# Kernel tuning notes

Measured on AMD Instinct MI355X. Metric: run time of the kernel, lower is better.

The kernel has to match this reference:

```python
import jax, jax.numpy as jnp
import numpy as np

B, L, D_MODEL, HEADS, EXP, DEPTH = 2, 2048, 1024, 16, 2, 12
D_EXP = D_MODEL * EXP
D_HEAD = D_EXP // HEADS


def _layernorm(x, g, b, eps=1e-5):
    mu = jnp.mean(x, axis=-1, keepdims=True)
    var = jnp.mean(jnp.square(x - mu), axis=-1, keepdims=True)
    return (x - mu) * jax.lax.rsqrt(var + eps) * g + b


def setup_inputs() -> dict:
    key = jax.random.key(0)
    ks = jax.random.split(key, 4)
    x = jax.random.normal(ks[0], (B, L, D_MODEL), dtype=jnp.float32)
    w_in = jax.random.normal(ks[1], (D_MODEL, 4 * D_EXP), dtype=jnp.float32) * 0.02
    w_out = jax.random.normal(ks[2], (D_EXP, D_MODEL), dtype=jnp.float32) * (0.02 / np.sqrt(2 * DEPTH))
    return {
        "x": x,
        "ln1_g": jnp.ones((D_MODEL,), jnp.float32),
        "ln1_b": jnp.zeros((D_MODEL,), jnp.float32),
        "ln2_g": jnp.ones((D_MODEL,), jnp.float32),
        "ln2_b": jnp.zeros((D_MODEL,), jnp.float32),
        "w_in": w_in,
        "w_out": w_out,
        "smear_factor": jnp.linspace(-6.0, 6.0, HEADS, dtype=jnp.float32),
        "log_scale": jnp.zeros((HEADS,), jnp.float32),
    }


def reference(x, ln1_g, ln1_b, ln2_g, ln2_b, w_in, w_out, smear_factor, log_scale):
    b, l, d = x.shape
    h = smear_factor.shape[0]
    d_exp = w_in.shape[1] // 4
    dh = d_exp // h

    qkvp = _layernorm(x, ln1_g, ln1_b) @ w_in  # [b, l, 4*d_exp]
    q, k, v, p = jnp.split(qkvp, 4, axis=-1)
    # 'b i (h d) -> b h i d'
    to_heads = lambda t: t.reshape(b, l, h, dh).transpose(0, 2, 1, 3)
    q, k, v = to_heads(q), to_heads(k), to_heads(v)

    # smeared keys: k_i <- (1-s)*k_i + s*k_{i-1}  (zero at i=0)
    smear = jax.nn.sigmoid(smear_factor)[None, :, None, None]
    k_prev = jnp.pad(k, ((0, 0), (0, 0), (1, 0), (0, 0)))[:, :, :-1, :]
    k = (1.0 - smear) * k + smear * k_prev

    # ALiBi-style additive mask: slope[h]*j on causal part, -1e10 above diag
    half = h // 2
    slopes = jnp.concatenate([2.0 ** jnp.linspace(0.0, -8.0, half), jnp.zeros((h - half,), jnp.float32)])
    j = jnp.arange(l)
    causal = jnp.where(j[None, :] > j[:, None], jnp.float32(-1e10), jnp.float32(0.0))  # [l, l]
    mask = slopes[:, None, None] * j[None, None, :].astype(jnp.float32) + causal[None, :, :]  # [h, l, l]

    # SDPA with q/s, k/s and default scale 1/sqrt(dh): logits = q k^T / (s^2 sqrt(dh))
    inv = 1.0 / (jnp.exp(2.0 * log_scale)[None, :, None, None] * jnp.sqrt(jnp.float32(dh)))
    logits = jnp.einsum('bhid,bhjd->bhij', q, k) * inv + mask[None]
    attn = jax.nn.softmax(logits, axis=-1)
    o = jnp.einsum('bhij,bhjd->bhid', attn, v)
    o = o.transpose(0, 2, 1, 3).reshape(b, l, h * dh)  # 'b h i d -> b i (h d)'

    out = (jax.nn.silu(p) * o) @ w_out
    return _layernorm(out, ln2_g, ln2_b)
```

## Files before the change

kernel.cpp:

```cpp
#include <hip/hip_runtime.h>

typedef unsigned short u16;
typedef __attribute__((ext_vector_type(8))) short bf16x8;
typedef __attribute__((ext_vector_type(8))) unsigned short u16x8;
typedef __attribute__((ext_vector_type(4))) float f32x4;

#define L_SEQ 2048
#define NTOK 4096
#define DMODEL 1024
#define DEXP 2048
#define NH 16
#define DH 128

__device__ __forceinline__ u16 f2bf(float f) {
    unsigned u = __float_as_uint(f);
    unsigned r = (u + 0x7FFFu + ((u >> 16) & 1u)) >> 16;
    return (u16)r;
}
__device__ __forceinline__ float bf2f(u16 h) {
    return __uint_as_float(((unsigned)h) << 16);
}

template <int CTRL>
__device__ __forceinline__ float dpp_f(float x) {
    return __int_as_float(__builtin_amdgcn_update_dpp(0, __float_as_int(x), CTRL, 0xF, 0xF, true));
}
__device__ __forceinline__ float red16_max(float x) {
    x = fmaxf(x, dpp_f<0xB1>(x));
    x = fmaxf(x, dpp_f<0x4E>(x));
    x = fmaxf(x, dpp_f<0x124>(x));
    x = fmaxf(x, dpp_f<0x128>(x));
    return x;
}

__device__ __forceinline__ void gl_lds16(const u16* g, u16* l) {
    __builtin_amdgcn_global_load_lds((const __attribute__((address_space(1))) void*)g,
                                     (__attribute__((address_space(3))) void*)l, 16, 0, 0);
}

__global__ void conv_transpose(const float* __restrict__ in, u16* __restrict__ out, int R, int C) {
    __shared__ unsigned tile[32][33];
    int c0 = blockIdx.x * 32, r0 = blockIdx.y * 32;
    int tx = threadIdx.x, ty = threadIdx.y;
    for (int j = 0; j < 32; j += 8)
        tile[ty + j][tx] = (unsigned)f2bf(in[(size_t)(r0 + ty + j) * C + c0 + tx]);
    __syncthreads();
    for (int j = 0; j < 32; j += 8)
        out[(size_t)(c0 + ty + j) * R + r0 + tx] = (u16)tile[tx][ty + j];
}

__global__ __launch_bounds__(256) void ln_fwd(const float* __restrict__ x, const float* __restrict__ g,
                                              const float* __restrict__ bta, void* __restrict__ outp,
                                              int out_bf16) {
    int row = blockIdx.x;
    int t = threadIdx.x;
    const float* xr = x + (size_t)row * DMODEL;
    float4 xv = *(const float4*)&xr[t * 4];
    float s = xv.x + xv.y + xv.z + xv.w;
    float s2 = xv.x * xv.x + xv.y * xv.y + xv.z * xv.z + xv.w * xv.w;
    for (int off = 32; off >= 1; off >>= 1) {
        s += __shfl_xor(s, off);
        s2 += __shfl_xor(s2, off);
    }
    __shared__ float red[10];
    int w = t >> 6;
    if ((t & 63) == 0) { red[w] = s; red[4 + w] = s2; }
    __syncthreads();
    if (t == 0) {
        red[8] = red[0] + red[1] + red[2] + red[3];
        red[9] = red[4] + red[5] + red[6] + red[7];
    }
    __syncthreads();
    float mu = red[8] * (1.0f / DMODEL);
    float var = red[9] * (1.0f / DMODEL) - mu * mu;
    float rstd = rsqrtf(var + 1e-5f);
    float vals[4] = {xv.x, xv.y, xv.z, xv.w};
    for (int e = 0; e < 4; e++) {
        int c = t * 4 + e;
        float y = (vals[e] - mu) * rstd * g[c] + bta[c];
        if (out_bf16) ((u16*)outp)[(size_t)row * DMODEL + c] = f2bf(y);
        else          ((float*)outp)[(size_t)row * DMODEL + c] = y;
    }
}

__device__ __forceinline__ void store_out(u16* C, size_t idx, float v) { C[idx] = f2bf(v); }
__device__ __forceinline__ void store_out(float* C, size_t idx, float v) { C[idx] = v; }

template <typename OutT>
__global__ __launch_bounds__(256) void gemm_bt(const u16* __restrict__ A, const u16* __restrict__ BT,
                                               OutT* __restrict__ C, int M, int N, int K) {
    __shared__ u16 a_s[2][4096];
    __shared__ u16 b_s[2][4096];
    int tid = threadIdx.x;
    unsigned NX = gridDim.x;
    unsigned lin = blockIdx.x + NX * blockIdx.y;
    unsigned per = NX >> 3;
    unsigned xcd = lin & 7, t = lin >> 3;
    unsigned n_p = xcd * per + (t % per);
    unsigned m_p = t / per;
    int m0 = m_p * 128, n0 = n_p * 128;
    int w = tid >> 6, lane = tid & 63, quad = lane >> 4, ln = lane & 15;
    int wr = (w >> 1) * 64, wc = (w & 1) * 64;
    f32x4 zero4 = {0.f, 0.f, 0.f, 0.f};
    f32x4 acc[4][4];
    for (int r = 0; r < 4; r++)
        for (int c = 0; c < 4; c++) acc[r][c] = zero4;

    int lrow = lane >> 2, lseg = (lane & 3) * 8;
    const u16* Ag0 = A + (size_t)(m0 + 32 * w + lrow) * K + lseg;
    const u16* Ag1 = Ag0 + (size_t)16 * K;
    const u16* Bg0 = BT + (size_t)(n0 + 32 * w + lrow) * K + lseg;
    const u16* Bg1 = Bg0 + (size_t)16 * K;
    int lo0 = (2 * w) * 512, lo1 = (2 * w + 1) * 512;

    gl_lds16(Ag0, &a_s[0][lo0]);
    gl_lds16(Ag1, &a_s[0][lo1]);
    gl_lds16(Bg0, &b_s[0][lo0]);
    gl_lds16(Bg1, &b_s[0][lo1]);
    __syncthreads();

    int cur = 0;
    for (int k0 = 0; k0 < K; k0 += 32) {
        if (k0 + 32 < K) {
            int nb = cur ^ 1;
            gl_lds16(Ag0 + k0 + 32, &a_s[nb][lo0]);
            gl_lds16(Ag1 + k0 + 32, &a_s[nb][lo1]);
            gl_lds16(Bg0 + k0 + 32, &b_s[nb][lo0]);
            gl_lds16(Bg1 + k0 + 32, &b_s[nb][lo1]);
        }
        bf16x8 af[4], bfr[4];
        for (int r = 0; r < 4; r++) af[r]  = *(const bf16x8*)&a_s[cur][(wr + r * 16 + ln) * 32 + quad * 8];
        for (int c = 0; c < 4; c++) bfr[c] = *(const bf16x8*)&b_s[cur][(wc + c * 16 + ln) * 32 + quad * 8];
        __builtin_amdgcn_s_setprio(1);
        for (int r = 0; r < 4; r++)
            for (int c = 0; c < 4; c++)
                acc[r][c] = __builtin_amdgcn_mfma_f32_16x16x32_bf16(af[r], bfr[c], acc[r][c], 0, 0, 0);
        __builtin_amdgcn_s_setprio(0);
        __syncthreads();
        cur ^= 1;
    }
    for (int r = 0; r < 4; r++)
        for (int c = 0; c < 4; c++)
            for (int e = 0; e < 4; e++) {
                int row = m0 + wr + r * 16 + quad * 4 + e;
                int col = n0 + wc + c * 16 + ln;
                store_out(C, (size_t)row * N + col, acc[r][c][e]);
            }
}

__global__ __launch_bounds__(256) void smear_kernel(const u16* __restrict__ qkvp,
                                                    const float* __restrict__ smear_f,
                                                    u16* __restrict__ k_sm) {
    int gid = blockIdx.x * 256 + threadIdx.x;
    int base = gid * 8;
    int bl = base >> 11;
    int c = base & 2047;
    int h = c >> 7;
    int d = c & 127;
    int l = bl & (L_SEQ - 1);
    int bb = bl >> 11;
    float s = 1.0f / (1.0f + __expf(-smear_f[h]));
    u16x8 cur = *(const u16x8*)&qkvp[(size_t)bl * 8192 + 2048 + c];
    u16x8 prv = {0, 0, 0, 0, 0, 0, 0, 0};
    if (l > 0) prv = *(const u16x8*)&qkvp[(size_t)(bl - 1) * 8192 + 2048 + c];
    u16x8 outv;
    for (int u = 0; u < 8; u++) {
        float kc = bf2f(cur[u]);
        float kp = bf2f(prv[u]);
        outv[u] = f2bf((1.0f - s) * kc + s * kp);
    }
    *(u16x8*)&k_sm[(((size_t)(bb * 16 + h)) * L_SEQ + l) * DH + d] = outv;
}

__global__ void vT_kernel(const u16* __restrict__ qkvp, u16* __restrict__ v_t) {
    __shared__ unsigned tile[32][33];
    int l0 = blockIdx.x * 32, d0 = blockIdx.y * 32;
    int bh = blockIdx.z;
    int bb = bh >> 4, h = bh & 15;
    int tx = threadIdx.x, ty = threadIdx.y;
    size_t tokb = (size_t)bb * L_SEQ;
    for (int j = 0; j < 32; j += 8)
        tile[ty + j][tx] = (unsigned)qkvp[(tokb + l0 + ty + j) * 8192 + 4096 + h * DH + d0 + tx];
    __syncthreads();
    for (int j = 0; j < 32; j += 8)
        v_t[((size_t)bh * DH + d0 + ty + j) * L_SEQ + l0 + tx] = (u16)tile[tx][ty + j];
}

__global__ __launch_bounds__(256) void attn_kernel(const u16* __restrict__ qkvp,
                                                   const u16* __restrict__ k_sm,
                                                   const u16* __restrict__ v_t,
                                                   u16* __restrict__ ag2,
                                                   const float* __restrict__ log_scale) {
    __shared__ u16 k_s[16384];
    __shared__ u16 vt_s[16384];
    __shared__ u16 p_s[4608];
    int tid = threadIdx.x;
    unsigned lin = blockIdx.x + 16u * blockIdx.y;
    unsigned xcd = lin & 7, tt = lin >> 3;
    int bh = (int)(xcd * 4 + (tt & 3));
    int pair = (int)(tt >> 2);
    int bb = bh >> 4, h = bh & 15;
    int w = tid >> 6, lane = tid & 63, quad = lane >> 4, ln = lane & 15;
    size_t tokb = (size_t)bb * L_SEQ;

    const float LOG2E = 1.44269504f;
    float inv = 1.0f / (__expf(2.0f * log_scale[h]) * sqrtf((float)DH));
    float scl = inv * LOG2E;
    float slope2 = ((h < 8) ? exp2f(-8.0f * (float)h / 7.0f) : 0.0f) * LOG2E;

    int lrow = lane >> 2, lcol = lane & 3;
    int lsw8 = (lcol ^ ((lrow >> 1) & 3)) * 8;
    int qsw = (quad ^ ((ln >> 1) & 3)) * 8;
    f32x4 zero4 = {0.f, 0.f, 0.f, 0.f};
    u16* pw = &p_s[w * 1152];
    const short ONE_BF = (short)0x3F80;
    bf16x8 ones = {ONE_BF, ONE_BF, ONE_BF, ONE_BF, ONE_BF, ONE_BF, ONE_BF, ONE_BF};

    for (int sidx = 0; sidx < 2; sidx++) {
        int ib = sidx == 0 ? (31 - pair) : pair;
        int i0 = ib * 64;
        int si = i0 + w * 16;

        bf16x8 qf[4];
        for (int kt = 0; kt < 4; kt++)
            qf[kt] = *(const bf16x8*)&qkvp[(tokb + si + ln) * 8192 + h * DH + kt * 32 + quad * 8];

        float m_i[4];
        for (int r = 0; r < 4; r++) m_i[r] = -1e30f;
        f32x4 o_acc[8], l_acc;
        for (int dt = 0; dt < 8; dt++) o_acc[dt] = zero4;
        l_acc = zero4;

        const u16* kg[4];
        for (int g = 0; g < 4; g++)
            kg[g] = k_sm + ((size_t)bh * L_SEQ + g * 16 + lrow) * DH + w * 32 + lsw8;
        const u16* vg[4];
        int vloff[4];
        for (int q = 0; q < 4; q++) {
            int c = w * 4 + q;
            int jt = c >> 3, dg = c & 7;
            vg[q] = v_t + ((size_t)bh * DH + dg * 16 + lrow) * L_SEQ + jt * 32 + lsw8;
            vloff[q] = jt * 4096 + dg * 512;
        }

        for (int g = 0; g < 4; g++) { gl_lds16(kg[g], &k_s[w * 2048 + g * 512]); kg[g] += 64 * DH; }
        for (int q = 0; q < 4; q++) { gl_lds16(vg[q], &vt_s[vloff[q]]); vg[q] += 64; }
        __syncthreads();

        int cur = 0;
        for (int j0 = 0; j0 <= i0; j0 += 64) {
            if (j0 + 64 <= i0) {
                int nb = (cur ^ 1) * 8192;
                for (int g = 0; g < 4; g++) { gl_lds16(kg[g], &k_s[nb + w * 2048 + g * 512]); kg[g] += 64 * DH; }
                for (int q = 0; q < 4; q++) { gl_lds16(vg[q], &vt_s[nb + vloff[q]]); vg[q] += 64; }
            }
            const u16* kb = &k_s[cur * 8192];
            const u16* vb = &vt_s[cur * 8192];

            f32x4 sc[4];
            for (int ct = 0; ct < 4; ct++) sc[ct] = zero4;
            __builtin_amdgcn_s_setprio(1);
            for (int kt = 0; kt < 4; kt++)
                for (int ct = 0; ct < 4; ct++) {
                    bf16x8 bfr = *(const bf16x8*)&kb[kt * 2048 + (ct * 16 + ln) * 32 + qsw];
                    sc[ct] = __builtin_amdgcn_mfma_f32_16x16x32_bf16(qf[kt], bfr, sc[ct], 0, 0, 0);
                }
            __builtin_amdgcn_s_setprio(0);

            bool full = (j0 + 63 <= si);
            float s2[4][4];
            float aj0 = slope2 * (float)(j0 + ln);
            for (int ct = 0; ct < 4; ct++) {
                float ajv = aj0 + slope2 * (float)(16 * ct);
                int j = j0 + ct * 16 + ln;
                for (int r = 0; r < 4; r++) {
                    float v = fmaf(sc[ct][r], scl, ajv);
                    if (!full) {
                        int i = si + quad * 4 + r;
                        if (j > i) v = -3.0e38f;
                    }
                    s2[ct][r] = v;
                }
            }
            float alpha[4];
            bool any_resc = false;
            for (int r = 0; r < 4; r++) {
                float mr = fmaxf(fmaxf(s2[0][r], s2[1][r]), fmaxf(s2[2][r], s2[3][r]));
                mr = red16_max(mr);
                float mnew = fmaxf(m_i[r], mr);
                alpha[r] = exp2f(m_i[r] - mnew);
                any_resc |= (alpha[r] != 1.0f);
                m_i[r] = mnew;
                for (int ct = 0; ct < 4; ct++) {
                    float p = exp2f(s2[ct][r] - mnew);
                    u16 pb = (u16)(__float_as_uint(p) >> 16);
                    pw[(quad * 4 + r) * 72 + ct * 16 + ln] = pb;
                }
            }
            if (__any(any_resc)) {
                for (int dt = 0; dt < 8; dt++) {
                    f32x4 o = o_acc[dt];
                    for (int r = 0; r < 4; r++) o[r] *= alpha[r];
                    o_acc[dt] = o;
                }
                for (int r = 0; r < 4; r++) l_acc[r] *= alpha[r];
            }
            asm volatile("s_waitcnt lgkmcnt(0)" ::: "memory");
            __builtin_amdgcn_s_setprio(1);
            for (int ks = 0; ks < 2; ks++) {
                bf16x8 pa = *(const bf16x8*)&pw[ln * 72 + ks * 32 + quad * 8];
                l_acc = __builtin_amdgcn_mfma_f32_16x16x32_bf16(pa, ones, l_acc, 0, 0, 0);
                for (int dt = 0; dt < 8; dt++) {
                    bf16x8 vf = *(const bf16x8*)&vb[ks * 4096 + (dt * 16 + ln) * 32 + qsw];
                    o_acc[dt] = __builtin_amdgcn_mfma_f32_16x16x32_bf16(pa, vf, o_acc[dt], 0, 0, 0);
                }
            }
            __builtin_amdgcn_s_setprio(0);
            __syncthreads();
            cur ^= 1;
        }

        float rinv[4];
        for (int r = 0; r < 4; r++) rinv[r] = __builtin_amdgcn_rcpf(l_acc[r]);
        for (int dt = 0; dt < 8; dt++)
            for (int r = 0; r < 4; r++) {
                int i = si + quad * 4 + r;
                int dcol = dt * 16 + ln;
                float o = o_acc[dt][r] * rinv[r];
                float pv = bf2f(qkvp[(tokb + i) * 8192 + 6144 + h * DH + dcol]);
                float gate = pv * __builtin_amdgcn_rcpf(1.0f + exp2f(-pv * LOG2E));
                ag2[(tokb + i) * 2048 + h * DH + dcol] = f2bf(gate * o);
            }
    }
}

extern "C" void kernel_launch(void* const* d_in, const int* in_sizes, int n_in,
                              void* d_out, int out_size, void* d_ws, size_t ws_size,
                              hipStream_t stream) {
    const float* x       = (const float*)d_in[0];
    const float* ln1_g   = (const float*)d_in[1];
    const float* ln1_b   = (const float*)d_in[2];
    const float* ln2_g   = (const float*)d_in[3];
    const float* ln2_b   = (const float*)d_in[4];
    const float* w_in    = (const float*)d_in[5];
    const float* w_out   = (const float*)d_in[6];
    const float* smear_f = (const float*)d_in[7];
    const float* logsc   = (const float*)d_in[8];
    float* out = (float*)d_out;
    char* ws = (char*)d_ws;

    u16* w_inT   = (u16*)(ws + 0);
    u16* w_outT  = (u16*)(ws + (size_t)16777216);
    u16* lnA     = (u16*)(ws + (size_t)20971520);
    u16* qkvp    = (u16*)(ws + (size_t)29360128);
    u16* k_sm    = (u16*)(ws + (size_t)96468992);
    u16* ag2     = (u16*)(ws + (size_t)113246208);
    float* out_pre = (float*)(ws + (size_t)96468992);
    u16* v_t     = (u16*)(ws + 0);

    dim3 b32x8(32, 8);
    conv_transpose<<<dim3(8192 / 32, 1024 / 32), b32x8, 0, stream>>>(w_in, w_inT, 1024, 8192);
    conv_transpose<<<dim3(1024 / 32, 2048 / 32), b32x8, 0, stream>>>(w_out, w_outT, 2048, 1024);
    ln_fwd<<<NTOK, 256, 0, stream>>>(x, ln1_g, ln1_b, (void*)lnA, 1);
    gemm_bt<u16><<<dim3(8192 / 128, 4096 / 128), 256, 0, stream>>>(lnA, w_inT, qkvp, NTOK, 8192, 1024);
    smear_kernel<<<4096, 256, 0, stream>>>(qkvp, smear_f, k_sm);
    vT_kernel<<<dim3(L_SEQ / 32, DH / 32, 32), b32x8, 0, stream>>>(qkvp, v_t);
    attn_kernel<<<dim3(16, 32), 256, 0, stream>>>(qkvp, k_sm, v_t, ag2, logsc);
    gemm_bt<float><<<dim3(1024 / 128, 4096 / 128), 256, 0, stream>>>(ag2, w_outT, out_pre, NTOK, 1024, 2048);
    ln_fwd<<<NTOK, 256, 0, stream>>>(out_pre, ln2_g, ln2_b, (void*)out, 0);
}
```

Before: 363.9 us.

## Replace input projection GEMM with 256x256-tile, 8-wave phased MFMA kernel

New measurement: 366.1 us. No clear change (+0.6%).

```diff
diff --git a/kernel.cpp b/kernel.cpp
--- a/kernel.cpp
+++ b/kernel.cpp
@@ -145,6 +145,122 @@
                 int row = m0 + wr + r * 16 + quad * 4 + e;
                 int col = n0 + wc + c * 16 + ln;
                 store_out(C, (size_t)row * N + col, acc[r][c][e]);
+            }
+}
+
+__global__ __launch_bounds__(512, 2) void gemm_8ph(const u16* __restrict__ A, const u16* __restrict__ BT,
+                                                   u16* __restrict__ C, int M, int N, int K) {
+    __shared__ u16 a_s[2][16384];
+    __shared__ u16 b_s[2][16384];
+    int tid = threadIdx.x;
+    int w = tid >> 6, lane = tid & 63, quad = lane >> 4, ln = lane & 15;
+    int wm = w >> 2, wn = w & 3;
+
+    unsigned lin = blockIdx.x + gridDim.x * blockIdx.y;
+    unsigned per = gridDim.x >> 3;
+    unsigned xcd = lin & 7, tt = lin >> 3;
+    unsigned n_p = xcd * per + (tt % per);
+    unsigned m_p = tt / per;
+    int m0 = m_p * 256, n0 = n_p * 256;
+
+    const u16* Asrc[4];
+    const u16* Bsrc[4];
+#pragma unroll
+    for (int j = 0; j < 4; j++) {
+        int s = j * 512 + tid;
+        int row = s >> 3, seg = s & 7;
+        int segx = seg ^ (row & 7);
+        Asrc[j] = A + (size_t)(m0 + row) * K + segx * 8;
+        Bsrc[j] = BT + (size_t)(n0 + row) * K + segx * 8;
+    }
+
+    f32x4 zero4 = {0.f, 0.f, 0.f, 0.f};
+    f32x4 acc[8][4];
+#pragma unroll
+    for (int m = 0; m < 8; m++)
+#pragma unroll
+        for (int n = 0; n < 4; n++) acc[m][n] = zero4;
+
+    bf16x8 af[4][2];
+    bf16x8 bfr[2][2];
+
+#define STAGE_G1(T, BUF)                                                              \
+    do {                                                                              \
+        _Pragma("unroll") for (int j = 0; j < 4; j++) {                               \
+            gl_lds16(Asrc[j] + (size_t)(T)*64, &a_s[BUF][(j * 512 + w * 64) * 8]);    \
+            gl_lds16(Bsrc[j] + (size_t)(T)*64, &b_s[BUF][(j * 512 + w * 64) * 8]);    \
+        }                                                                             \
+    } while (0)
+
+#define LOADA_G1(BUF, QM)                                                             \
+    do {                                                                              \
+        _Pragma("unroll") for (int mt = 0; mt < 4; mt++)                              \
+        _Pragma("unroll") for (int kt = 0; kt < 2; kt++)                              \
+            af[mt][kt] = *(const bf16x8*)&a_s[BUF][(wm * 128 + (QM)*64 + mt * 16 + ln) * 64 + \
+                                                   (((kt * 4 + quad) ^ (ln & 7)) * 8)];       \
+    } while (0)
+
+#define LOADB_G1(BUF, QN)                                                             \
+    do {                                                                              \
+        _Pragma("unroll") for (int nt = 0; nt < 2; nt++)                              \
+        _Pragma("unroll") for (int kt = 0; kt < 2; kt++)                              \
+            bfr[nt][kt] = *(const bf16x8*)&b_s[BUF][(wn * 64 + (QN)*32 + nt * 16 + ln) * 64 + \
+                                                    (((kt * 4 + quad) ^ (ln & 7)) * 8)];      \
+    } while (0)
+
+#define MFMA_G1(QM, QN)                                                               \
+    do {                                                                              \
+        __builtin_amdgcn_s_barrier();                                                 \
+        __builtin_amdgcn_s_setprio(1);                                                \
+        _Pragma("unroll") for (int mt = 0; mt < 4; mt++)                              \
+        _Pragma("unroll") for (int nt = 0; nt < 2; nt++)                              \
+        _Pragma("unroll") for (int kt = 0; kt < 2; kt++)                              \
+            acc[(QM)*4 + mt][(QN)*2 + nt] = __builtin_amdgcn_mfma_f32_16x16x32_bf16(  \
+                af[mt][kt], bfr[nt][kt], acc[(QM)*4 + mt][(QN)*2 + nt], 0, 0, 0);     \
+        __builtin_amdgcn_s_setprio(0);                                                \
+        __builtin_amdgcn_s_barrier();                                                 \
+    } while (0)
+
+    int NT = K >> 6;
+    STAGE_G1(0, 0);
+    STAGE_G1(1, 1);
+    asm volatile("s_waitcnt vmcnt(8)" ::: "memory");
+    __builtin_amdgcn_s_barrier();
+
+    for (int t = 0; t < NT; t++) {
+        int buf = t & 1;
+        LOADA_G1(buf, 0);
+        LOADB_G1(buf, 0);
+        MFMA_G1(0, 0);
+        LOADB_G1(buf, 1);
+        MFMA_G1(0, 1);
+        LOADA_G1(buf, 1);
+        MFMA_G1(1, 1);
+        LOADB_G1(buf, 0);
+        MFMA_G1(1, 0);
+        if (t + 2 < NT) {
+            STAGE_G1(t + 2, buf);
+            asm volatile("s_waitcnt vmcnt(8)" ::: "memory");
+        } else {
+            asm volatile("s_waitcnt vmcnt(0)" ::: "memory");
+        }
+        __builtin_amdgcn_s_barrier();
+    }
+
+#undef STAGE_G1
+#undef LOADA_G1
+#undef LOADB_G1
+#undef MFMA_G1
+
+#pragma unroll
+    for (int m = 0; m < 8; m++)
+#pragma unroll
+        for (int n = 0; n < 4; n++)
+#pragma unroll
+            for (int e = 0; e < 4; e++) {
+                int row = m0 + wm * 128 + m * 16 + quad * 4 + e;
+                int col = n0 + wn * 64 + n * 16 + ln;
+                C[(size_t)row * N + col] = f2bf(acc[m][n][e]);
             }
 }
 
@@ -362,7 +478,7 @@
     conv_transpose<<<dim3(8192 / 32, 1024 / 32), b32x8, 0, stream>>>(w_in, w_inT, 1024, 8192);
     conv_transpose<<<dim3(1024 / 32, 2048 / 32), b32x8, 0, stream>>>(w_out, w_outT, 2048, 1024);
     ln_fwd<<<NTOK, 256, 0, stream>>>(x, ln1_g, ln1_b, (void*)lnA, 1);
-    gemm_bt<u16><<<dim3(8192 / 128, 4096 / 128), 256, 0, stream>>>(lnA, w_inT, qkvp, NTOK, 8192, 1024);
+    gemm_8ph<<<dim3(8192 / 256, 4096 / 256), 512, 0, stream>>>(lnA, w_inT, qkvp, NTOK, 8192, 1024);
     smear_kernel<<<4096, 256, 0, stream>>>(qkvp, smear_f, k_sm);
     vT_kernel<<<dim3(L_SEQ / 32, DH / 32, 32), b32x8, 0, stream>>>(qkvp, v_t);
     attn_kernel<<<dim3(16, 32), 256, 0, stream>>>(qkvp, k_sm, v_t, ag2, logsc);
```

## Software-pipeline attention PV matmul one tile behind QK with double-buffered P

Applied to the files above, without the earlier changes.

Result: slower. 435.7 us (+19.7%).

```diff
diff --git a/kernel.cpp b/kernel.cpp
--- a/kernel.cpp
+++ b/kernel.cpp
@@ -193,7 +193,7 @@
                                                    const float* __restrict__ log_scale) {
     __shared__ u16 k_s[16384];
     __shared__ u16 vt_s[16384];
-    __shared__ u16 p_s[4608];
+    __shared__ u16 p_s[2][4096];
     int tid = threadIdx.x;
     unsigned lin = blockIdx.x + 16u * blockIdx.y;
     unsigned xcd = lin & 7, tt = lin >> 3;
@@ -212,7 +212,8 @@
     int lsw8 = (lcol ^ ((lrow >> 1) & 3)) * 8;
     int qsw = (quad ^ ((ln >> 1) & 3)) * 8;
     f32x4 zero4 = {0.f, 0.f, 0.f, 0.f};
-    u16* pw = &p_s[w * 1152];
+    u16* pwA = &p_s[0][w * 1024];
+    u16* pwB = &p_s[1][w * 1024];
     const short ONE_BF = (short)0x3F80;
     bf16x8 ones = {ONE_BF, ONE_BF, ONE_BF, ONE_BF, ONE_BF, ONE_BF, ONE_BF, ONE_BF};
 
@@ -220,6 +221,7 @@
         int ib = sidx == 0 ? (31 - pair) : pair;
         int i0 = ib * 64;
         int si = i0 + w * 16;
+        int nt = i0 >> 6;
 
         bf16x8 qf[4];
         for (int kt = 0; kt < 4; kt++)
@@ -244,18 +246,19 @@
         }
 
         for (int g = 0; g < 4; g++) { gl_lds16(kg[g], &k_s[w * 2048 + g * 512]); kg[g] += 64 * DH; }
-        for (int q = 0; q < 4; q++) { gl_lds16(vg[q], &vt_s[vloff[q]]); vg[q] += 64; }
         __syncthreads();
 
-        int cur = 0;
-        for (int j0 = 0; j0 <= i0; j0 += 64) {
-            if (j0 + 64 <= i0) {
-                int nb = (cur ^ 1) * 8192;
+        for (int t = 0; t <= nt; t++) {
+            int j0 = t << 6;
+            if (t < nt) {
+                int nb = ((t + 1) & 1) * 8192;
                 for (int g = 0; g < 4; g++) { gl_lds16(kg[g], &k_s[nb + w * 2048 + g * 512]); kg[g] += 64 * DH; }
-                for (int q = 0; q < 4; q++) { gl_lds16(vg[q], &vt_s[nb + vloff[q]]); vg[q] += 64; }
-            }
-            const u16* kb = &k_s[cur * 8192];
-            const u16* vb = &vt_s[cur * 8192];
+            }
+            {
+                int vb_ = (t & 1) * 8192;
+                for (int q = 0; q < 4; q++) { gl_lds16(vg[q], &vt_s[vb_ + vloff[q]]); vg[q] += 64; }
+            }
+            const u16* kb = &k_s[(t & 1) * 8192];
 
             f32x4 sc[4];
             for (int ct = 0; ct < 4; ct++) sc[ct] = zero4;
@@ -266,6 +269,21 @@
                     sc[ct] = __builtin_amdgcn_mfma_f32_16x16x32_bf16(qf[kt], bfr, sc[ct], 0, 0, 0);
                 }
             __builtin_amdgcn_s_setprio(0);
+
+            if (t > 0) {
+                const u16* vbp = &vt_s[((t - 1) & 1) * 8192];
+                const u16* pr = (t & 1) ? pwA : pwB;
+                __builtin_amdgcn_s_setprio(1);
+                for (int ks = 0; ks < 2; ks++) {
+                    bf16x8 pa = *(const bf16x8*)&pr[ln * 64 + (((ks * 4 + quad) ^ (ln & 7)) << 3)];
+                    l_acc = __builtin_amdgcn_mfma_f32_16x16x32_bf16(pa, ones, l_acc, 0, 0, 0);
+                    for (int dt = 0; dt < 8; dt++) {
+                        bf16x8 vf = *(const bf16x8*)&vbp[ks * 4096 + (dt * 16 + ln) * 32 + qsw];
+                        o_acc[dt] = __builtin_amdgcn_mfma_f32_16x16x32_bf16(pa, vf, o_acc[dt], 0, 0, 0);
+                    }
+                }
+                __builtin_amdgcn_s_setprio(0);
+            }
 
             bool full = (j0 + 63 <= si);
             float s2[4][4];
@@ -282,6 +300,7 @@
                     s2[ct][r] = v;
                 }
             }
+            u16* pcur = (t & 1) ? pwB : pwA;
             float alpha[4];
             bool any_resc = false;
             for (int r = 0; r < 4; r++) {
@@ -291,10 +310,13 @@
                 alpha[r] = exp2f(m_i[r] - mnew);
                 any_resc |= (alpha[r] != 1.0f);
                 m_i[r] = mnew;
+                int row = quad * 4 + r;
+                int rk = row & 7;
                 for (int ct = 0; ct < 4; ct++) {
                     float p = exp2f(s2[ct][r] - mnew);
                     u16 pb = (u16)(__float_as_uint(p) >> 16);
-                    pw[(quad * 4 + r) * 72 + ct * 16 + ln] = pb;
+                    int sl = ct * 2 + (ln >> 3);
+                    pcur[row * 64 + ((sl ^ rk) << 3) + (ln & 7)] = pb;
                 }
             }
             if (__any(any_resc)) {
@@ -305,19 +327,22 @@
                 }
                 for (int r = 0; r < 4; r++) l_acc[r] *= alpha[r];
             }
-            asm volatile("s_waitcnt lgkmcnt(0)" ::: "memory");
+            __syncthreads();
+        }
+
+        {
+            const u16* vbp = &vt_s[(nt & 1) * 8192];
+            const u16* pr = (nt & 1) ? pwB : pwA;
             __builtin_amdgcn_s_setprio(1);
             for (int ks = 0; ks < 2; ks++) {
-                bf16x8 pa = *(const bf16x8*)&pw[ln * 72 + ks * 32 + quad * 8];
+                bf16x8 pa = *(const bf16x8*)&pr[ln * 64 + (((ks * 4 + quad) ^ (ln & 7)) << 3)];
                 l_acc = __builtin_amdgcn_mfma_f32_16x16x32_bf16(pa, ones, l_acc, 0, 0, 0);
                 for (int dt = 0; dt < 8; dt++) {
-                    bf16x8 vf = *(const bf16x8*)&vb[ks * 4096 + (dt * 16 + ln) * 32 + qsw];
+                    bf16x8 vf = *(const bf16x8*)&vbp[ks * 4096 + (dt * 16 + ln) * 32 + qsw];
                     o_acc[dt] = __builtin_amdgcn_mfma_f32_16x16x32_bf16(pa, vf, o_acc[dt], 0, 0, 0);
                 }
             }
             __builtin_amdgcn_s_setprio(0);
-            __syncthreads();
-            cur ^= 1;
         }
 
         float rinv[4];
```
